# Kernel optimization log

Hardware: AMD Instinct MI355X
Metric: run time of the kernel (lower is better)

Reference implementation:

```python
import jax, jax.numpy as jnp
import numpy as np

N, E, S = 50000, 800000, 3          # nodes, edges, message-passing steps
ND, ED, GD = 7, 4, 2                # raw node/edge/global feature dims
H, L = 64, 64                       # hidden and latent sizes


def _mlp3(x, W0, b0, W1, b1, W2, b2):
    # MLP([H, H, L]) with gelu between layers, none after last (dropout off).
    x = jax.nn.gelu(x @ W0 + b0)
    x = jax.nn.gelu(x @ W1 + b1)
    return x @ W2 + b2


def _ln(x, scale, bias, eps=1e-6):
    mu = jnp.mean(x, axis=-1, keepdims=True)
    xc = x - mu
    var = jnp.mean(xc * xc, axis=-1, keepdims=True)
    return xc * jax.lax.rsqrt(var + eps) * scale + bias


def setup_inputs() -> dict:
    key = jax.random.key(0)
    ks = iter(jax.random.split(key, 40))

    def W(i, o, stacked=False):
        shape = (S, i, o) if stacked else (i, o)
        return (jax.random.normal(next(ks), shape, jnp.float32) / np.sqrt(i)).astype(jnp.float32)

    inp = {
        "nodes": jax.random.normal(next(ks), (N, ND), jnp.float32),
        "edges": jax.random.normal(next(ks), (E, ED), jnp.float32),
        "glob": jax.random.normal(next(ks), (1, GD), jnp.float32),
        # node embedder MLP [H,H,L]
        "emb_n_W0": W(ND, H), "emb_n_b0": jnp.zeros((H,), jnp.float32),
        "emb_n_W1": W(H, H), "emb_n_b1": jnp.zeros((H,), jnp.float32),
        "emb_n_W2": W(H, L), "emb_n_b2": jnp.zeros((L,), jnp.float32),
        # edge embedder MLP
        "emb_e_W0": W(ED, H), "emb_e_b0": jnp.zeros((H,), jnp.float32),
        "emb_e_W1": W(H, H), "emb_e_b1": jnp.zeros((H,), jnp.float32),
        "emb_e_W2": W(H, L), "emb_e_b2": jnp.zeros((L,), jnp.float32),
        # per-step edge update MLP: in = edges(L)+senders(L)+receivers(L)+glob(GD)
        "edge_W0": W(3 * L + GD, H, True), "edge_b0": jnp.zeros((S, H), jnp.float32),
        "edge_W1": W(H, H, True), "edge_b1": jnp.zeros((S, H), jnp.float32),
        "edge_W2": W(H, L, True), "edge_b2": jnp.zeros((S, L), jnp.float32),
        # per-step node update MLP: in = nodes(L)+received(L)+glob(GD)
        "node_W0": W(2 * L + GD, H, True), "node_b0": jnp.zeros((S, H), jnp.float32),
        "node_W1": W(H, H, True), "node_b1": jnp.zeros((S, H), jnp.float32),
        "node_W2": W(H, L, True), "node_b2": jnp.zeros((S, L), jnp.float32),
        # per-step LayerNorms for nodes and edges
        "ln_n_scale": jnp.ones((S, L), jnp.float32), "ln_n_bias": jnp.zeros((S, L), jnp.float32),
        "ln_e_scale": jnp.ones((S, L), jnp.float32), "ln_e_bias": jnp.zeros((S, L), jnp.float32),
        # decoder MLP [H,H,3]
        "dec_W0": W(L, H), "dec_b0": jnp.zeros((H,), jnp.float32),
        "dec_W1": W(H, H), "dec_b1": jnp.zeros((H,), jnp.float32),
        "dec_W2": W(H, 3), "dec_b2": jnp.zeros((3,), jnp.float32),
        "senders": jax.random.randint(next(ks), (E,), 0, N),
        "receivers": jax.random.randint(next(ks), (E,), 0, N),
    }
    return inp


def reference(nodes, edges, glob,
              emb_n_W0, emb_n_b0, emb_n_W1, emb_n_b1, emb_n_W2, emb_n_b2,
              emb_e_W0, emb_e_b0, emb_e_W1, emb_e_b1, emb_e_W2, emb_e_b2,
              edge_W0, edge_b0, edge_W1, edge_b1, edge_W2, edge_b2,
              node_W0, node_b0, node_W1, node_b1, node_W2, node_b2,
              ln_n_scale, ln_n_bias, ln_e_scale, ln_e_bias,
              dec_W0, dec_b0, dec_W1, dec_b1, dec_W2, dec_b2,
              senders, receivers):
    # GraphMapFeatures embedder
    n = _mlp3(nodes, emb_n_W0, emb_n_b0, emb_n_W1, emb_n_b1, emb_n_W2, emb_n_b2)  # [N, L]
    e = _mlp3(edges, emb_e_W0, emb_e_b0, emb_e_W1, emb_e_b1, emb_e_W2, emb_e_b2)  # [E, L]
    n_nodes, n_edges = n.shape[0], e.shape[0]
    ge = jnp.broadcast_to(glob, (n_edges, glob.shape[1]))  # globals per edge (single graph)
    gn = jnp.broadcast_to(glob, (n_nodes, glob.shape[1]))  # globals per node
    steps = edge_W0.shape[0]
    for s in range(steps):
        # edge update: gather sender/receiver node feats, concat, MLP
        e_in = jnp.concatenate([e, n[senders], n[receivers], ge], axis=1)  # [E, 3L+GD]
        new_e = _mlp3(e_in, edge_W0[s], edge_b0[s], edge_W1[s], edge_b1[s], edge_W2[s], edge_b2[s])
        # scatter-aggregate to receivers (jraph default: segment_sum)
        recv = jax.ops.segment_sum(new_e, receivers, num_segments=n_nodes)  # [N, L]
        n_in = jnp.concatenate([n, recv, gn], axis=1)  # [N, 2L+GD]
        new_n = _mlp3(n_in, node_W0[s], node_b0[s], node_W1[s], node_b1[s], node_W2[s], node_b2[s])
        # residual skip connections then per-step LayerNorm
        n = _ln(n + new_n, ln_n_scale[s], ln_n_bias[s])
        e = _ln(e + new_e, ln_e_scale[s], ln_e_bias[s])
    # decoder on nodes -> [N, 3]
    return _mlp3(n, dec_W0, dec_b0, dec_W1, dec_b1, dec_W2, dec_b2)
```

## Files before the change

kernel.cpp:

```cpp
#include <hip/hip_runtime.h>

#define N_NODES 50000
#define N_EDGES 800000
#define NSTEPS 3
#define NBLK_SCAN 196

typedef __attribute__((ext_vector_type(8))) short bf16x8;
typedef __attribute__((ext_vector_type(4))) float f32x4;


__device__ __forceinline__ float ldf(const void* p, long i, int bf) {
    if (bf) {
        unsigned int u = ((const unsigned short*)p)[i];
        u <<= 16;
        return __uint_as_float(u);
    }
    return ((const float*)p)[i];
}

__device__ __forceinline__ unsigned short f2bf(float f) {
    return (unsigned short)((__float_as_uint(f) + 0x8000u) >> 16);
}

__device__ __forceinline__ float bf2f(unsigned short u) {
    return __uint_as_float(((unsigned int)u) << 16);
}

__device__ __forceinline__ float gelu_f(float x) {
    float x2 = x * x;
    float m = x * fmaf(-0.10294325f, x2, -2.30220847f);
    float e = __builtin_amdgcn_exp2f(m);
    return x * __builtin_amdgcn_rcpf(1.0f + e);
}

__device__ __forceinline__ void zero4(f32x4 a[4]) {
#pragma unroll
    for (int t = 0; t < 4; t++) a[t] = (f32x4){0.f, 0.f, 0.f, 0.f};
}

__device__ __forceinline__ void mfma_chunk(f32x4 acc[4], bf16x8 a, const unsigned short* bb) {
    acc[0] = __builtin_amdgcn_mfma_f32_16x16x32_bf16(a, *(const bf16x8*)(bb + 0), acc[0], 0, 0, 0);
    acc[1] = __builtin_amdgcn_mfma_f32_16x16x32_bf16(a, *(const bf16x8*)(bb + 512), acc[1], 0, 0, 0);
    acc[2] = __builtin_amdgcn_mfma_f32_16x16x32_bf16(a, *(const bf16x8*)(bb + 1024), acc[2], 0, 0, 0);
    acc[3] = __builtin_amdgcn_mfma_f32_16x16x32_bf16(a, *(const bf16x8*)(bb + 1536), acc[3], 0, 0, 0);
}

__global__ void detect_kernel(const void* probe, int* flag) {
    if (threadIdx.x == 0 && blockIdx.x == 0) {
        unsigned int w = *(const unsigned int*)probe;
        *flag = (w == 0x3F803F80u) ? 1 : 0;
    }
}

__global__ void hist_kernel(const int* __restrict__ receivers, int* __restrict__ counts) {
    int i = blockIdx.x * 256 + threadIdx.x;
    if (i < N_EDGES) atomicAdd(&counts[receivers[i]], 1);
}

__global__ void scan_partial(const int* __restrict__ counts, int* __restrict__ base,
                             int* __restrict__ blockSums) {
    __shared__ int sm[256];
    int b = blockIdx.x, t = threadIdx.x, i = b * 256 + t;
    int v = (i < N_NODES) ? counts[i] : 0;
    sm[t] = v;
    __syncthreads();
    for (int off = 1; off < 256; off <<= 1) {
        int x = (t >= off) ? sm[t - off] : 0;
        __syncthreads();
        sm[t] += x;
        __syncthreads();
    }
    if (i < N_NODES) base[i] = sm[t] - v;
    if (t == 255) blockSums[b] = sm[255];
}

__global__ void scan_tops(int* __restrict__ blockSums, int* __restrict__ tops) {
    __shared__ int sm[256];
    int t = threadIdx.x;
    int v = (t < NBLK_SCAN) ? blockSums[t] : 0;
    sm[t] = v;
    __syncthreads();
    for (int off = 1; off < 256; off <<= 1) {
        int x = (t >= off) ? sm[t - off] : 0;
        __syncthreads();
        sm[t] += x;
        __syncthreads();
    }
    if (t < NBLK_SCAN) tops[t] = sm[t] - v;
}

__global__ void scan_add(int* __restrict__ base, const int* __restrict__ tops,
                         int* __restrict__ cursor) {
    int b = blockIdx.x, i = b * 256 + threadIdx.x;
    if (i < N_NODES) {
        int v = base[i] + tops[b];
        base[i] = v;
        cursor[i] = v;
    }
}

__global__ void scatter_kernel(const int* __restrict__ senders,
                               const int* __restrict__ receivers, int* __restrict__ cursor,
                               int* __restrict__ ss, int* __restrict__ rsrt,
                               int* __restrict__ perm) {
    int i = blockIdx.x * 256 + threadIdx.x;
    if (i < N_EDGES) {
        int r = receivers[i];
        int pos = atomicAdd(&cursor[r], 1);
        ss[pos] = senders[i];
        rsrt[pos] = r;
        perm[pos] = i;
    }
}

struct PrepPtrs {
    const void* W[14];
    const void* eb0;
    const void* nb0;
    const void* glob;
};

#define PREP_WTOTAL 139264
__global__ void prep_all(PrepPtrs p, unsigned short* WbBase, float* b0eff_e, float* b0eff_n,
                         const int* __restrict__ flagp) {
    const int totals[14] = {36864, 12288, 12288, 24576, 12288, 12288, 2048,
                            4096,  4096,  2048,  4096,  4096,  4096,  4096};
    const int ksrc[14] = {192, 64, 64, 128, 64, 64, 7, 64, 64, 4, 64, 64, 64, 64};
    const int sstride[14] = {12416, 4096, 4096, 8320, 4096, 4096, 448,
                             4096,  4096, 256,  4096, 4096, 4096, 4096};
    const int nch[14] = {6, 2, 2, 4, 2, 2, 1, 2, 2, 1, 2, 2, 2, 2};

    const int bf = *flagp;
    int i = blockIdx.x * 256 + threadIdx.x;
    if (i < PREP_WTOTAL) {
        int e = 0, base = 0;
        while (i >= base + totals[e]) { base += totals[e]; e++; }
        int il = i - base;
        int j = il & 7, lane = (il >> 3) & 63, t = (il >> 9) & 3;
        int c = (il >> 11) % nch[e], s = il / (2048 * nch[e]);
        int k = c * 32 + (lane >> 4) * 8 + j;
        int col = t * 16 + (lane & 15);
        WbBase[i] = (k < ksrc[e]) ? f2bf(ldf(p.W[e], (long)s * sstride[e] + (long)k * 64 + col, bf))
                                  : (unsigned short)0;
    } else if (i < PREP_WTOTAL + 384) {
        int i2 = i - PREP_WTOTAL;
        float g0 = ldf(p.glob, 0, bf), g1 = ldf(p.glob, 1, bf);
        if (i2 < 192) {
            int s = i2 >> 6, col = i2 & 63;
            b0eff_e[i2] = ldf(p.eb0, i2, bf) + g0 * ldf(p.W[0], (long)s * 12416 + 192 * 64 + col, bf)
                                             + g1 * ldf(p.W[0], (long)s * 12416 + 193 * 64 + col, bf);
        } else {
            int il = i2 - 192;
            int s = il >> 6, col = il & 63;
            b0eff_n[il] = ldf(p.nb0, il, bf) + g0 * ldf(p.W[3], (long)s * 8320 + 128 * 64 + col, bf)
                                             + g1 * ldf(p.W[3], (long)s * 8320 + 129 * 64 + col, bf);
        }
    }
}

template <int DIN, int OUT_BF>
__global__ __launch_bounds__(256) void embed_mfma(
    const void* __restrict__ xin, const unsigned short* __restrict__ Wb0, const void* b0,
    const unsigned short* __restrict__ Wb1, const void* b1,
    const unsigned short* __restrict__ Wb2, const void* b2, void* __restrict__ outp,
    unsigned short* __restrict__ out_bf, const int* __restrict__ perm, int R,
    const int* __restrict__ flagp) {
    __shared__ __align__(16) unsigned short Xs[64 * 40];
    __shared__ __align__(16) unsigned short hbuf[64 * 72];
    const int bf = *flagp;
    const int tid = threadIdx.x;
    const long rb = (long)blockIdx.x * 64;
    const int lane = tid & 63, w = tid >> 6, q = lane >> 4, l15 = lane & 15;
    const int arow = 16 * w + l15, aoff = q * 8;
    unsigned short* hw = hbuf + w * 16 * 72;

    {
        int r = tid >> 2, seg = tid & 3;
        long idx = rb + r;
        long src = (perm != nullptr && idx < R) ? (long)perm[idx] : idx;
        unsigned short u[8];
#pragma unroll
        for (int j = 0; j < 8; j++) {
            int col = seg * 8 + j;
            u[j] = (col < DIN && idx < R) ? f2bf(ldf(xin, src * DIN + col, bf)) : (unsigned short)0;
        }
        *(uint4*)&Xs[r * 40 + seg * 8] = *(uint4*)u;
    }

    f32x4 acc[4];
    zero4(acc);
    {
        bf16x8 a = *(const bf16x8*)&Xs[arow * 40 + aoff];
        mfma_chunk(acc, a, Wb0 + lane * 8);
#pragma unroll
        for (int t = 0; t < 4; t++) {
            int col = t * 16 + l15;
            float b = ldf(b0, col, bf);
#pragma unroll
            for (int reg = 0; reg < 4; reg++)
                hw[(q * 4 + reg) * 72 + col] = f2bf(gelu_f(acc[t][reg] + b));
        }
    }
    zero4(acc);
    {
#pragma unroll
        for (int c = 0; c < 2; c++) {
            bf16x8 a = *(const bf16x8*)&hw[l15 * 72 + c * 32 + aoff];
            mfma_chunk(acc, a, Wb1 + c * 2048 + lane * 8);
        }
#pragma unroll
        for (int t = 0; t < 4; t++) {
            int col = t * 16 + l15;
            float b = ldf(b1, col, bf);
#pragma unroll
            for (int reg = 0; reg < 4; reg++)
                hw[(q * 4 + reg) * 72 + col] = f2bf(gelu_f(acc[t][reg] + b));
        }
    }
    zero4(acc);
    {
#pragma unroll
        for (int c = 0; c < 2; c++) {
            bf16x8 a = *(const bf16x8*)&hw[l15 * 72 + c * 32 + aoff];
            mfma_chunk(acc, a, Wb2 + c * 2048 + lane * 8);
        }
    }
    if (OUT_BF) {
#pragma unroll
        for (int t = 0; t < 4; t++) {
            int col = t * 16 + l15;
            float b = ldf(b2, col, bf);
#pragma unroll
            for (int reg = 0; reg < 4; reg++)
                hw[(q * 4 + reg) * 72 + col] = f2bf(acc[t][reg] + b);
        }
#pragma unroll
        for (int p = 0; p < 2; p++) {
            int r = 16 * w + p * 8 + (lane >> 3), o = lane & 7;
            long idx = rb + r;
            if (idx < R)
                *(uint4*)&((unsigned short*)outp)[idx * 64 + o * 8] =
                    *(const uint4*)&hbuf[r * 72 + o * 8];
        }
    } else {
#pragma unroll
        for (int t = 0; t < 4; t++) {
            int col = t * 16 + l15;
            float b = ldf(b2, col, bf);
#pragma unroll
            for (int reg = 0; reg < 4; reg++) {
                long idx = rb + 16 * w + q * 4 + reg;
                if (idx < R) {
                    float v = acc[t][reg] + b;
                    ((float*)outp)[idx * 64 + col] = v;
                    out_bf[idx * 64 + col] = f2bf(v);
                }
            }
        }
    }
}

#define EST 72
#define NST 68
__global__ __launch_bounds__(256) void edge_update_mfma(
    unsigned short* __restrict__ e_lat, const unsigned short* __restrict__ n_bf,
    const int* __restrict__ ss, const int* __restrict__ rsrt,
    const unsigned short* __restrict__ Wb0, const unsigned short* __restrict__ Wb1,
    const unsigned short* __restrict__ Wb2, const float* __restrict__ b0eff, const void* b1,
    const void* b2, const void* lnsc, const void* lnbi, float* __restrict__ recvbuf, int s,
    const int* __restrict__ flagp) {
    __shared__ __align__(16) unsigned short Ee[64 * EST];
    __shared__ __align__(16) unsigned short NsNr[128 * NST];
    __shared__ int rcvs[64];
    float* newe = (float*)NsNr;

    const int bf = *flagp;
    const int tid = threadIdx.x;
    const long rb = (long)blockIdx.x * 64;
    const int lane = tid & 63, w = tid >> 6, q = lane >> 4, l15 = lane & 15;
    const int arow = 16 * w + l15, aoff = q * 8;
    unsigned short* hw = Ee + w * 16 * EST;

#pragma unroll
    for (int p = 0; p < 2; p++) {
        int r = 16 * w + p * 8 + (lane >> 3), o = lane & 7;
        *(uint4*)&Ee[r * EST + o * 8] = ((const uint4*)(e_lat + (rb + r) * 64))[o];
    }
#pragma unroll
    for (int p = 0; p < 2; p++) {
        int r = 16 * w + p * 8 + (lane >> 3), o = lane & 7;
        long node = ss[rb + r];
        *(uint4*)&NsNr[r * NST + o * 8] = ((const uint4*)(n_bf + node * 64))[o];
    }
#pragma unroll
    for (int p = 0; p < 2; p++) {
        int r = 16 * w + p * 8 + (lane >> 3), o = lane & 7;
        long node = rsrt[rb + r];
        *(uint4*)&NsNr[(64 + r) * NST + o * 8] = ((const uint4*)(n_bf + node * 64))[o];
    }
    if (lane < 16) rcvs[16 * w + lane] = rsrt[rb + 16 * w + lane];

    float ein[4][4];
#pragma unroll
    for (int reg = 0; reg < 4; reg++)
#pragma unroll
        for (int t = 0; t < 4; t++)
            ein[reg][t] = bf2f(Ee[(16 * w + q * 4 + reg) * EST + t * 16 + l15]);

    f32x4 acc[4];
    zero4(acc);
    {
        const unsigned short* B = Wb0 + (long)s * 6 * 2048 + lane * 8;
#pragma unroll
        for (int c = 0; c < 2; c++) {
            bf16x8 a = *(const bf16x8*)&Ee[arow * EST + c * 32 + aoff];
            mfma_chunk(acc, a, B + c * 2048);
        }
#pragma unroll
        for (int c = 0; c < 2; c++) {
            bf16x8 a = *(const bf16x8*)&NsNr[arow * NST + c * 32 + aoff];
            mfma_chunk(acc, a, B + (2 + c) * 2048);
        }
#pragma unroll
        for (int c = 0; c < 2; c++) {
            bf16x8 a = *(const bf16x8*)&NsNr[(64 + arow) * NST + c * 32 + aoff];
            mfma_chunk(acc, a, B + (4 + c) * 2048);
        }
#pragma unroll
        for (int t = 0; t < 4; t++) {
            const int col = t * 16 + l15;
            const float b = b0eff[s * 64 + col];
#pragma unroll
            for (int reg = 0; reg < 4; reg++)
                hw[(q * 4 + reg) * EST + col] = f2bf(gelu_f(acc[t][reg] + b));
        }
    }
    zero4(acc);
    {
        const unsigned short* B = Wb1 + (long)s * 2 * 2048 + lane * 8;
#pragma unroll
        for (int c = 0; c < 2; c++) {
            bf16x8 a = *(const bf16x8*)&hw[l15 * EST + c * 32 + aoff];
            mfma_chunk(acc, a, B + c * 2048);
        }
#pragma unroll
        for (int t = 0; t < 4; t++) {
            const int col = t * 16 + l15;
            const float b = ldf(b1, (long)s * 64 + col, bf);
#pragma unroll
            for (int reg = 0; reg < 4; reg++)
                hw[(q * 4 + reg) * EST + col] = f2bf(gelu_f(acc[t][reg] + b));
        }
    }
    zero4(acc);
    {
        const unsigned short* B = Wb2 + (long)s * 2 * 2048 + lane * 8;
#pragma unroll
        for (int c = 0; c < 2; c++) {
            bf16x8 a = *(const bf16x8*)&hw[l15 * EST + c * 32 + aoff];
            mfma_chunk(acc, a, B + c * 2048);
        }
    }
    __syncthreads();

    float fin[4][4];
#pragma unroll
    for (int t = 0; t < 4; t++) {
        const float b = ldf(b2, (long)s * 64 + t * 16 + l15, bf);
#pragma unroll
        for (int reg = 0; reg < 4; reg++) fin[reg][t] = acc[t][reg] + b;
    }
    float lsc[4], lbi[4];
#pragma unroll
    for (int t = 0; t < 4; t++) {
        lsc[t] = ldf(lnsc, (long)s * 64 + t * 16 + l15, bf);
        lbi[t] = ldf(lnbi, (long)s * 64 + t * 16 + l15, bf);
    }
#pragma unroll
    for (int reg = 0; reg < 4; reg++) {
        const int lr = q * 4 + reg;
        float u[4], ssum = 0.f;
#pragma unroll
        for (int t = 0; t < 4; t++) {
            newe[w * 1056 + lr * 66 + t * 16 + l15] = fin[reg][t];
            u[t] = ein[reg][t] + fin[reg][t];
            ssum += u[t];
        }
#pragma unroll
        for (int m = 1; m < 16; m <<= 1) ssum += __shfl_xor(ssum, m, 64);
        const float mu = ssum * (1.0f / 64.0f);
        float d[4], vv = 0.f;
#pragma unroll
        for (int t = 0; t < 4; t++) { d[t] = u[t] - mu; vv += d[t] * d[t]; }
#pragma unroll
        for (int m = 1; m < 16; m <<= 1) vv += __shfl_xor(vv, m, 64);
        const float rs = rsqrtf(vv * (1.0f / 64.0f) + 1e-6f);
#pragma unroll
        for (int t = 0; t < 4; t++)
            Ee[(16 * w + lr) * EST + t * 16 + l15] = f2bf(d[t] * rs * lsc[t] + lbi[t]);
    }

#pragma unroll
    for (int p = 0; p < 2; p++) {
        int r = 16 * w + p * 8 + (lane >> 3), o = lane & 7;
        *(uint4*)&e_lat[(rb + r) * 64 + o * 8] = *(const uint4*)&Ee[r * EST + o * 8];
    }
    {
        const int col = tid & 63, g = tid >> 6;
        float a = 0.f;
#pragma unroll
        for (int rr = 0; rr < 16; rr++) {
            const int r = 16 * g + rr;
            a += newe[g * 1056 + rr * 66 + col];
            if (rr == 15 || rcvs[r + 1] != rcvs[r]) {
                atomicAdd(&recvbuf[(long)rcvs[r] * 64 + col], a);
                a = 0.f;
            }
        }
    }
}

#define NXS 136
__global__ __launch_bounds__(256) void node_update_mfma(
    float* __restrict__ n_lat, unsigned short* __restrict__ n_bf, float* __restrict__ recvbuf,
    const unsigned short* __restrict__ Wb0, const float* __restrict__ b0eff,
    const unsigned short* __restrict__ Wb1, const void* b1,
    const unsigned short* __restrict__ Wb2, const void* b2, const void* lnsc,
    const void* lnbi, int s, const int* __restrict__ flagp) {
    __shared__ __align__(16) unsigned short Xs[64 * NXS];
    __shared__ __align__(16) unsigned short hbuf[64 * 72];
    const int bf = *flagp;
    const int tid = threadIdx.x;
    const long rb = (long)blockIdx.x * 64;
    const int lane = tid & 63, w = tid >> 6, q = lane >> 4, l15 = lane & 15;
    const int arow = 16 * w + l15, aoff = q * 8;
    unsigned short* hw = hbuf + w * 16 * 72;

#pragma unroll
    for (int p = 0; p < 2; p++) {
        int r = 16 * w + p * 8 + (lane >> 3), o = lane & 7;
        long idx = rb + r;
        uint4 v = {0u, 0u, 0u, 0u};
        if (idx < N_NODES) v = ((const uint4*)(n_bf + idx * 64))[o];
        *(uint4*)&Xs[r * NXS + o * 8] = v;
    }
#pragma unroll
    for (int p = 0; p < 2; p++) {
        int r = 16 * w + p * 8 + (lane >> 3), o = lane & 7;
        long idx = rb + r;
        unsigned short u[8] = {0, 0, 0, 0, 0, 0, 0, 0};
        if (idx < N_NODES) {
            const float* src = recvbuf + idx * 64 + o * 8;
            float4 x0 = *(const float4*)src, x1 = *(const float4*)(src + 4);
            u[0] = f2bf(x0.x); u[1] = f2bf(x0.y); u[2] = f2bf(x0.z); u[3] = f2bf(x0.w);
            u[4] = f2bf(x1.x); u[5] = f2bf(x1.y); u[6] = f2bf(x1.z); u[7] = f2bf(x1.w);
        }
        *(uint4*)&Xs[r * NXS + 64 + o * 8] = *(uint4*)u;
    }

    f32x4 acc[4];
    zero4(acc);
    {
        const unsigned short* B = Wb0 + (long)s * 4 * 2048 + lane * 8;
#pragma unroll
        for (int c = 0; c < 4; c++) {
            bf16x8 a = *(const bf16x8*)&Xs[arow * NXS + c * 32 + aoff];
            mfma_chunk(acc, a, B + c * 2048);
        }
#pragma unroll
        for (int t = 0; t < 4; t++) {
            const int col = t * 16 + l15;
            const float b = b0eff[s * 64 + col];
#pragma unroll
            for (int reg = 0; reg < 4; reg++)
                hw[(q * 4 + reg) * 72 + col] = f2bf(gelu_f(acc[t][reg] + b));
        }
    }
    zero4(acc);
    {
        const unsigned short* B = Wb1 + (long)s * 2 * 2048 + lane * 8;
#pragma unroll
        for (int c = 0; c < 2; c++) {
            bf16x8 a = *(const bf16x8*)&hw[l15 * 72 + c * 32 + aoff];
            mfma_chunk(acc, a, B + c * 2048);
        }
#pragma unroll
        for (int t = 0; t < 4; t++) {
            const int col = t * 16 + l15;
            const float b = ldf(b1, (long)s * 64 + col, bf);
#pragma unroll
            for (int reg = 0; reg < 4; reg++)
                hw[(q * 4 + reg) * 72 + col] = f2bf(gelu_f(acc[t][reg] + b));
        }
    }
    zero4(acc);
    {
        const unsigned short* B = Wb2 + (long)s * 2 * 2048 + lane * 8;
#pragma unroll
        for (int c = 0; c < 2; c++) {
            bf16x8 a = *(const bf16x8*)&hw[l15 * 72 + c * 32 + aoff];
            mfma_chunk(acc, a, B + c * 2048);
        }
    }
    float b2v[4], lsc[4], lbi[4];
#pragma unroll
    for (int t = 0; t < 4; t++) {
        b2v[t] = ldf(b2, (long)s * 64 + t * 16 + l15, bf);
        lsc[t] = ldf(lnsc, (long)s * 64 + t * 16 + l15, bf);
        lbi[t] = ldf(lnbi, (long)s * 64 + t * 16 + l15, bf);
    }
#pragma unroll
    for (int reg = 0; reg < 4; reg++) {
        const int rowl = 16 * w + q * 4 + reg;
        const long idx = rb + rowl;
        const bool valid = idx < N_NODES;
        float u[4], ssum = 0.f;
#pragma unroll
        for (int t = 0; t < 4; t++) {
            const int col = t * 16 + l15;
            float xn = valid ? n_lat[idx * 64 + col] : 0.f;
            u[t] = xn + acc[t][reg] + b2v[t];
            ssum += u[t];
        }
#pragma unroll
        for (int m = 1; m < 16; m <<= 1) ssum += __shfl_xor(ssum, m, 64);
        const float mu = ssum * (1.0f / 64.0f);
        float d[4], vv = 0.f;
#pragma unroll
        for (int t = 0; t < 4; t++) { d[t] = u[t] - mu; vv += d[t] * d[t]; }
#pragma unroll
        for (int m = 1; m < 16; m <<= 1) vv += __shfl_xor(vv, m, 64);
        const float rs = rsqrtf(vv * (1.0f / 64.0f) + 1e-6f);
        if (valid) {
#pragma unroll
            for (int t = 0; t < 4; t++) {
                const int col = t * 16 + l15;
                float v = d[t] * rs * lsc[t] + lbi[t];
                n_lat[idx * 64 + col] = v;
                n_bf[idx * 64 + col] = f2bf(v);
                recvbuf[idx * 64 + col] = 0.f;
            }
        }
    }
}

__global__ __launch_bounds__(256) void decoder_mfma(
    const unsigned short* __restrict__ n_bf, const unsigned short* __restrict__ Wb0,
    const void* b0, const unsigned short* __restrict__ Wb1, const void* b1, const void* W2,
    const void* b2, void* __restrict__ outp, const int* __restrict__ flagp) {
    __shared__ __align__(16) unsigned short Xs[64 * 72];
    __shared__ __align__(16) unsigned short hbuf[64 * 72];
    const int bf = *flagp;
    const int tid = threadIdx.x;
    const long rb = (long)blockIdx.x * 64;
    const int lane = tid & 63, w = tid >> 6, q = lane >> 4, l15 = lane & 15;
    const int arow = 16 * w + l15, aoff = q * 8;
    unsigned short* hw = hbuf + w * 16 * 72;

#pragma unroll
    for (int p = 0; p < 2; p++) {
        int r = 16 * w + p * 8 + (lane >> 3), o = lane & 7;
        long idx = rb + r;
        uint4 v = {0u, 0u, 0u, 0u};
        if (idx < N_NODES) v = ((const uint4*)(n_bf + idx * 64))[o];
        *(uint4*)&Xs[r * 72 + o * 8] = v;
    }

    f32x4 acc[4];
    zero4(acc);
    {
#pragma unroll
        for (int c = 0; c < 2; c++) {
            bf16x8 a = *(const bf16x8*)&Xs[arow * 72 + c * 32 + aoff];
            mfma_chunk(acc, a, Wb0 + c * 2048 + lane * 8);
        }
#pragma unroll
        for (int t = 0; t < 4; t++) {
            const int col = t * 16 + l15;
            const float b = ldf(b0, col, bf);
#pragma unroll
            for (int reg = 0; reg < 4; reg++)
                hw[(q * 4 + reg) * 72 + col] = f2bf(gelu_f(acc[t][reg] + b));
        }
    }
    zero4(acc);
    {
#pragma unroll
        for (int c = 0; c < 2; c++) {
            bf16x8 a = *(const bf16x8*)&hw[l15 * 72 + c * 32 + aoff];
            mfma_chunk(acc, a, Wb1 + c * 2048 + lane * 8);
        }
#pragma unroll
        for (int t = 0; t < 4; t++) {
            const int col = t * 16 + l15;
            const float b = ldf(b1, col, bf);
#pragma unroll
            for (int reg = 0; reg < 4; reg++)
                hw[(q * 4 + reg) * 72 + col] = f2bf(gelu_f(acc[t][reg] + b));
        }
    }
    const int col = tid & 63;
    const int r0 = (tid >> 6) * 16;
    if (col < 3) {
        float a[16];
        const float b = ldf(b2, col, bf);
#pragma unroll
        for (int i = 0; i < 16; i++) a[i] = b;
        for (int k = 0; k < 64; k++) {
            float wv = ldf(W2, (long)k * 3 + col, bf);
#pragma unroll
            for (int i = 0; i < 16; i++) a[i] = fmaf(bf2f(hbuf[(r0 + i) * 72 + k]), wv, a[i]);
        }
        for (int i = 0; i < 16; i++) {
            const long idx = rb + r0 + i;
            if (idx < N_NODES) {
                if (bf)
                    ((unsigned short*)outp)[idx * 3 + col] = f2bf(a[i]);
                else
                    ((float*)outp)[idx * 3 + col] = a[i];
            }
        }
    }
}

extern "C" void kernel_launch(void* const* d_in, const int* in_sizes, int n_in, void* d_out,
                              int out_size, void* d_ws, size_t ws_size, hipStream_t stream) {
    const void* nodes = d_in[0];
    const void* edges = d_in[1];
    const void* glob = d_in[2];
    const void *enW0 = d_in[3], *enb0 = d_in[4], *enW1 = d_in[5], *enb1 = d_in[6],
               *enW2 = d_in[7], *enb2 = d_in[8];
    const void *eeW0 = d_in[9], *eeb0 = d_in[10], *eeW1 = d_in[11], *eeb1 = d_in[12],
               *eeW2 = d_in[13], *eeb2 = d_in[14];
    const void *eW0 = d_in[15], *eb0 = d_in[16], *eW1 = d_in[17], *eb1 = d_in[18],
               *eW2 = d_in[19], *eb2 = d_in[20];
    const void *nW0 = d_in[21], *nb0 = d_in[22], *nW1 = d_in[23], *nb1 = d_in[24],
               *nW2 = d_in[25], *nb2 = d_in[26];
    const void *lnns = d_in[27], *lnnb = d_in[28], *lnes = d_in[29], *lneb = d_in[30];
    const void *dW0 = d_in[31], *db0 = d_in[32], *dW1 = d_in[33], *db1 = d_in[34],
               *dW2 = d_in[35], *db2 = d_in[36];
    const int* senders = (const int*)d_in[37];
    const int* receivers = (const int*)d_in[38];

    float* n_lat = (float*)d_ws;
    float* recvb = n_lat + 3200000;
    float* b0eff_e = recvb + 3200000;
    float* b0eff_n = b0eff_e + 192;
    int* flag = (int*)(b0eff_n + 192);
    unsigned short* e_lat = (unsigned short*)(b0eff_n + 256);
    unsigned short* n_bf = e_lat + 51200000;
    unsigned short* WbBase = n_bf + 3200000;
    unsigned short* WbE0 = WbBase;
    unsigned short* WbE1 = WbBase + 36864;
    unsigned short* WbE2 = WbBase + 49152;
    unsigned short* WbN0 = WbBase + 61440;
    unsigned short* WbN1 = WbBase + 86016;
    unsigned short* WbN2 = WbBase + 98304;
    unsigned short* WbNE0 = WbBase + 110592;
    unsigned short* WbNE1 = WbBase + 112640;
    unsigned short* WbNE2 = WbBase + 116736;
    unsigned short* WbEE0 = WbBase + 120832;
    unsigned short* WbEE1 = WbBase + 122880;
    unsigned short* WbEE2 = WbBase + 126976;
    unsigned short* WbD0 = WbBase + 131072;
    unsigned short* WbD1 = WbBase + 135168;
    int* counts = (int*)(WbBase + 139264 + 64);
    int* sbase = counts + N_NODES;
    int* cursor = sbase + N_NODES;
    int* blockSums = cursor + N_NODES;
    int* tops = blockSums + 256;
    int* ss = tops + 256;
    int* rsrt = ss + N_EDGES;
    int* perm = rsrt + N_EDGES;

    detect_kernel<<<1, 64, 0, stream>>>(lnns, flag);

    PrepPtrs pp;
    pp.W[0] = eW0;  pp.W[1] = eW1;  pp.W[2] = eW2;
    pp.W[3] = nW0;  pp.W[4] = nW1;  pp.W[5] = nW2;
    pp.W[6] = enW0; pp.W[7] = enW1; pp.W[8] = enW2;
    pp.W[9] = eeW0; pp.W[10] = eeW1; pp.W[11] = eeW2;
    pp.W[12] = dW0; pp.W[13] = dW1;
    pp.eb0 = eb0; pp.nb0 = nb0; pp.glob = glob;
    prep_all<<<(PREP_WTOTAL + 384 + 255) / 256, 256, 0, stream>>>(pp, WbBase, b0eff_e, b0eff_n,
                                                                  flag);
    hipMemsetAsync(recvb, 0, (size_t)N_NODES * 64 * sizeof(float), stream);
    hipMemsetAsync(counts, 0, (size_t)N_NODES * sizeof(int), stream);

    hist_kernel<<<(N_EDGES + 255) / 256, 256, 0, stream>>>(receivers, counts);
    scan_partial<<<NBLK_SCAN, 256, 0, stream>>>(counts, sbase, blockSums);
    scan_tops<<<1, 256, 0, stream>>>(blockSums, tops);
    scan_add<<<NBLK_SCAN, 256, 0, stream>>>(sbase, tops, cursor);
    scatter_kernel<<<(N_EDGES + 255) / 256, 256, 0, stream>>>(senders, receivers, cursor, ss,
                                                              rsrt, perm);

    embed_mfma<7, 0><<<(N_NODES + 63) / 64, 256, 0, stream>>>(
        nodes, WbNE0, enb0, WbNE1, enb1, WbNE2, enb2, n_lat, n_bf, (const int*)nullptr,
        N_NODES, flag);
    embed_mfma<4, 1><<<N_EDGES / 64, 256, 0, stream>>>(
        edges, WbEE0, eeb0, WbEE1, eeb1, WbEE2, eeb2, e_lat, (unsigned short*)nullptr, perm,
        N_EDGES, flag);
    for (int s = 0; s < NSTEPS; s++) {
        edge_update_mfma<<<N_EDGES / 64, 256, 0, stream>>>(
            e_lat, n_bf, ss, rsrt, WbE0, WbE1, WbE2, b0eff_e, eb1, eb2, lnes, lneb, recvb, s,
            flag);
        node_update_mfma<<<(N_NODES + 63) / 64, 256, 0, stream>>>(
            n_lat, n_bf, recvb, WbN0, b0eff_n, WbN1, nb1, WbN2, nb2, lnns, lnnb, s, flag);
    }
    decoder_mfma<<<(N_NODES + 63) / 64, 256, 0, stream>>>(n_bf, WbD0, db0, WbD1, db1, dW2,
                                                          db2, d_out, flag);
}
```

Before: 772.9 us.

## Fuse edge embedder into first edge step and decoder into last node step

The edge embedding MLP now runs inside the first edge-update kernel, so the embedded edge latents are never written to and re-read from global memory. The final edge step skips its LayerNorm and e_lat write-back, since those edge latents are never used again. The decoder is folded into the last node-update kernel. Sender and receiver node features are now loaded straight into MFMA operand registers instead of being staged through shared memory, which frees LDS and removes a __syncthreads. The cost is more template variants and higher register pressure in the fused kernels.

```diff
diff --git a/kernel.cpp b/kernel.cpp
--- a/kernel.cpp
+++ b/kernel.cpp
@@ -261,18 +261,20 @@
 }
 
 #define EST 72
-#define NST 68
-__global__ __launch_bounds__(256) void edge_update_mfma(
+template <int S0, int LAST>
+__global__ __launch_bounds__(256) void edge_step(
     unsigned short* __restrict__ e_lat, const unsigned short* __restrict__ n_bf,
-    const int* __restrict__ ss, const int* __restrict__ rsrt,
+    const int* __restrict__ ss, const int* __restrict__ rsrt, const int* __restrict__ perm,
+    const void* __restrict__ xe_raw, const unsigned short* __restrict__ We0, const void* eb0_,
+    const unsigned short* __restrict__ We1, const void* eb1_,
+    const unsigned short* __restrict__ We2, const void* eb2_,
     const unsigned short* __restrict__ Wb0, const unsigned short* __restrict__ Wb1,
     const unsigned short* __restrict__ Wb2, const float* __restrict__ b0eff, const void* b1,
     const void* b2, const void* lnsc, const void* lnbi, float* __restrict__ recvbuf, int s,
     const int* __restrict__ flagp) {
     __shared__ __align__(16) unsigned short Ee[64 * EST];
-    __shared__ __align__(16) unsigned short NsNr[128 * NST];
+    __shared__ __align__(16) float newe[4 * 1056];
     __shared__ int rcvs[64];
-    float* newe = (float*)NsNr;
 
     const int bf = *flagp;
     const int tid = threadIdx.x;
@@ -281,33 +283,86 @@
     const int arow = 16 * w + l15, aoff = q * 8;
     unsigned short* hw = Ee + w * 16 * EST;
 
-#pragma unroll
-    for (int p = 0; p < 2; p++) {
-        int r = 16 * w + p * 8 + (lane >> 3), o = lane & 7;
-        *(uint4*)&Ee[r * EST + o * 8] = ((const uint4*)(e_lat + (rb + r) * 64))[o];
-    }
-#pragma unroll
-    for (int p = 0; p < 2; p++) {
-        int r = 16 * w + p * 8 + (lane >> 3), o = lane & 7;
-        long node = ss[rb + r];
-        *(uint4*)&NsNr[r * NST + o * 8] = ((const uint4*)(n_bf + node * 64))[o];
-    }
-#pragma unroll
-    for (int p = 0; p < 2; p++) {
-        int r = 16 * w + p * 8 + (lane >> 3), o = lane & 7;
-        long node = rsrt[rb + r];
-        *(uint4*)&NsNr[(64 + r) * NST + o * 8] = ((const uint4*)(n_bf + node * 64))[o];
-    }
+    const int sn = ss[rb + arow], rn = rsrt[rb + arow];
+    const bf16x8 as0 = *(const bf16x8*)(n_bf + (long)sn * 64 + aoff);
+    const bf16x8 as1 = *(const bf16x8*)(n_bf + (long)sn * 64 + 32 + aoff);
+    const bf16x8 ar0 = *(const bf16x8*)(n_bf + (long)rn * 64 + aoff);
+    const bf16x8 ar1 = *(const bf16x8*)(n_bf + (long)rn * 64 + 32 + aoff);
     if (lane < 16) rcvs[16 * w + lane] = rsrt[rb + 16 * w + lane];
 
     float ein[4][4];
-#pragma unroll
-    for (int reg = 0; reg < 4; reg++)
-#pragma unroll
-        for (int t = 0; t < 4; t++)
-            ein[reg][t] = bf2f(Ee[(16 * w + q * 4 + reg) * EST + t * 16 + l15]);
-
     f32x4 acc[4];
+
+    if (S0) {
+        zero4(acc);
+        {
+            bf16x8 a = (bf16x8){0, 0, 0, 0, 0, 0, 0, 0};
+            if (q == 0) {
+                long src = perm[rb + arow];
+                unsigned short u[8] = {0, 0, 0, 0, 0, 0, 0, 0};
+#pragma unroll
+                for (int j = 0; j < 4; j++) u[j] = f2bf(ldf(xe_raw, src * 4 + j, bf));
+                a = *(const bf16x8*)u;
+            }
+            mfma_chunk(acc, a, We0 + lane * 8);
+#pragma unroll
+            for (int t = 0; t < 4; t++) {
+                int col = t * 16 + l15;
+                float b = ldf(eb0_, col, bf);
+#pragma unroll
+                for (int reg = 0; reg < 4; reg++)
+                    hw[(q * 4 + reg) * EST + col] = f2bf(gelu_f(acc[t][reg] + b));
+            }
+        }
+        zero4(acc);
+        {
+#pragma unroll
+            for (int c = 0; c < 2; c++) {
+                bf16x8 a = *(const bf16x8*)&hw[l15 * EST + c * 32 + aoff];
+                mfma_chunk(acc, a, We1 + c * 2048 + lane * 8);
+            }
+#pragma unroll
+            for (int t = 0; t < 4; t++) {
+                int col = t * 16 + l15;
+                float b = ldf(eb1_, col, bf);
+#pragma unroll
+                for (int reg = 0; reg < 4; reg++)
+                    hw[(q * 4 + reg) * EST + col] = f2bf(gelu_f(acc[t][reg] + b));
+            }
+        }
+        zero4(acc);
+        {
+#pragma unroll
+            for (int c = 0; c < 2; c++) {
+                bf16x8 a = *(const bf16x8*)&hw[l15 * EST + c * 32 + aoff];
+                mfma_chunk(acc, a, We2 + c * 2048 + lane * 8);
+            }
+#pragma unroll
+            for (int t = 0; t < 4; t++) {
+                int col = t * 16 + l15;
+                float b = ldf(eb2_, col, bf);
+#pragma unroll
+                for (int reg = 0; reg < 4; reg++) {
+                    ein[reg][t] = acc[t][reg] + b;
+                    Ee[(16 * w + q * 4 + reg) * EST + col] = f2bf(ein[reg][t]);
+                }
+            }
+        }
+    } else {
+#pragma unroll
+        for (int p = 0; p < 2; p++) {
+            int r = 16 * w + p * 8 + (lane >> 3), o = lane & 7;
+            *(uint4*)&Ee[r * EST + o * 8] = ((const uint4*)(e_lat + (rb + r) * 64))[o];
+        }
+        if (!LAST) {
+#pragma unroll
+            for (int reg = 0; reg < 4; reg++)
+#pragma unroll
+                for (int t = 0; t < 4; t++)
+                    ein[reg][t] = bf2f(Ee[(16 * w + q * 4 + reg) * EST + t * 16 + l15]);
+        }
+    }
+
     zero4(acc);
     {
         const unsigned short* B = Wb0 + (long)s * 6 * 2048 + lane * 8;
@@ -316,16 +371,10 @@
             bf16x8 a = *(const bf16x8*)&Ee[arow * EST + c * 32 + aoff];
             mfma_chunk(acc, a, B + c * 2048);
         }
-#pragma unroll
-        for (int c = 0; c < 2; c++) {
-            bf16x8 a = *(const bf16x8*)&NsNr[arow * NST + c * 32 + aoff];
-            mfma_chunk(acc, a, B + (2 + c) * 2048);
-        }
-#pragma unroll
-        for (int c = 0; c < 2; c++) {
-            bf16x8 a = *(const bf16x8*)&NsNr[(64 + arow) * NST + c * 32 + aoff];
-            mfma_chunk(acc, a, B + (4 + c) * 2048);
-        }
+        mfma_chunk(acc, as0, B + 2 * 2048);
+        mfma_chunk(acc, as1, B + 3 * 2048);
+        mfma_chunk(acc, ar0, B + 4 * 2048);
+        mfma_chunk(acc, ar1, B + 5 * 2048);
 #pragma unroll
         for (int t = 0; t < 4; t++) {
             const int col = t * 16 + l15;
@@ -361,7 +410,6 @@
             mfma_chunk(acc, a, B + c * 2048);
         }
     }
-    __syncthreads();
 
     float fin[4][4];
 #pragma unroll
@@ -371,39 +419,46 @@
         for (int reg = 0; reg < 4; reg++) fin[reg][t] = acc[t][reg] + b;
     }
     float lsc[4], lbi[4];
-#pragma unroll
-    for (int t = 0; t < 4; t++) {
-        lsc[t] = ldf(lnsc, (long)s * 64 + t * 16 + l15, bf);
-        lbi[t] = ldf(lnbi, (long)s * 64 + t * 16 + l15, bf);
+    if (!LAST) {
+#pragma unroll
+        for (int t = 0; t < 4; t++) {
+            lsc[t] = ldf(lnsc, (long)s * 64 + t * 16 + l15, bf);
+            lbi[t] = ldf(lnbi, (long)s * 64 + t * 16 + l15, bf);
+        }
     }
 #pragma unroll
     for (int reg = 0; reg < 4; reg++) {
         const int lr = q * 4 + reg;
-        float u[4], ssum = 0.f;
-#pragma unroll
-        for (int t = 0; t < 4; t++) {
-            newe[w * 1056 + lr * 66 + t * 16 + l15] = fin[reg][t];
-            u[t] = ein[reg][t] + fin[reg][t];
-            ssum += u[t];
-        }
-#pragma unroll
-        for (int m = 1; m < 16; m <<= 1) ssum += __shfl_xor(ssum, m, 64);
-        const float mu = ssum * (1.0f / 64.0f);
-        float d[4], vv = 0.f;
-#pragma unroll
-        for (int t = 0; t < 4; t++) { d[t] = u[t] - mu; vv += d[t] * d[t]; }
-#pragma unroll
-        for (int m = 1; m < 16; m <<= 1) vv += __shfl_xor(vv, m, 64);
-        const float rs = rsqrtf(vv * (1.0f / 64.0f) + 1e-6f);
-#pragma unroll
-        for (int t = 0; t < 4; t++)
-            Ee[(16 * w + lr) * EST + t * 16 + l15] = f2bf(d[t] * rs * lsc[t] + lbi[t]);
-    }
-
-#pragma unroll
-    for (int p = 0; p < 2; p++) {
-        int r = 16 * w + p * 8 + (lane >> 3), o = lane & 7;
-        *(uint4*)&e_lat[(rb + r) * 64 + o * 8] = *(const uint4*)&Ee[r * EST + o * 8];
+#pragma unroll
+        for (int t = 0; t < 4; t++) newe[w * 1056 + lr * 66 + t * 16 + l15] = fin[reg][t];
+        if (!LAST) {
+            float u[4], ssum = 0.f;
+#pragma unroll
+            for (int t = 0; t < 4; t++) {
+                u[t] = ein[reg][t] + fin[reg][t];
+                ssum += u[t];
+            }
+#pragma unroll
+            for (int m = 1; m < 16; m <<= 1) ssum += __shfl_xor(ssum, m, 64);
+            const float mu = ssum * (1.0f / 64.0f);
+            float d[4], vv = 0.f;
+#pragma unroll
+            for (int t = 0; t < 4; t++) { d[t] = u[t] - mu; vv += d[t] * d[t]; }
+#pragma unroll
+            for (int m = 1; m < 16; m <<= 1) vv += __shfl_xor(vv, m, 64);
+            const float rs = rsqrtf(vv * (1.0f / 64.0f) + 1e-6f);
+#pragma unroll
+            for (int t = 0; t < 4; t++)
+                Ee[(16 * w + lr) * EST + t * 16 + l15] = f2bf(d[t] * rs * lsc[t] + lbi[t]);
+        }
+    }
+
+    if (!LAST) {
+#pragma unroll
+        for (int p = 0; p < 2; p++) {
+            int r = 16 * w + p * 8 + (lane >> 3), o = lane & 7;
+            *(uint4*)&e_lat[(rb + r) * 64 + o * 8] = *(const uint4*)&Ee[r * EST + o * 8];
+        }
     }
     {
         const int col = tid & 63, g = tid >> 6;
@@ -421,12 +476,15 @@
 }
 
 #define NXS 136
+template <int FINAL>
 __global__ __launch_bounds__(256) void node_update_mfma(
     float* __restrict__ n_lat, unsigned short* __restrict__ n_bf, float* __restrict__ recvbuf,
     const unsigned short* __restrict__ Wb0, const float* __restrict__ b0eff,
     const unsigned short* __restrict__ Wb1, const void* b1,
     const unsigned short* __restrict__ Wb2, const void* b2, const void* lnsc,
-    const void* lnbi, int s, const int* __restrict__ flagp) {
+    const void* lnbi, const unsigned short* __restrict__ WbD0, const void* db0,
+    const unsigned short* __restrict__ WbD1, const void* db1, const void* dW2,
+    const void* db2, void* __restrict__ outp, int s, const int* __restrict__ flagp) {
     __shared__ __align__(16) unsigned short Xs[64 * NXS];
     __shared__ __align__(16) unsigned short hbuf[64 * 72];
     const int bf = *flagp;
@@ -531,7 +589,13 @@
 #pragma unroll
         for (int m = 1; m < 16; m <<= 1) vv += __shfl_xor(vv, m, 64);
         const float rs = rsqrtf(vv * (1.0f / 64.0f) + 1e-6f);
-        if (valid) {
+        if (FINAL) {
+#pragma unroll
+            for (int t = 0; t < 4; t++) {
+                const int col = t * 16 + l15;
+                hw[(q * 4 + reg) * 72 + col] = f2bf(d[t] * rs * lsc[t] + lbi[t]);
+            }
+        } else if (valid) {
 #pragma unroll
             for (int t = 0; t < 4; t++) {
                 const int col = t * 16 + l15;
@@ -542,82 +606,59 @@
             }
         }
     }
-}
-
-__global__ __launch_bounds__(256) void decoder_mfma(
-    const unsigned short* __restrict__ n_bf, const unsigned short* __restrict__ Wb0,
-    const void* b0, const unsigned short* __restrict__ Wb1, const void* b1, const void* W2,
-    const void* b2, void* __restrict__ outp, const int* __restrict__ flagp) {
-    __shared__ __align__(16) unsigned short Xs[64 * 72];
-    __shared__ __align__(16) unsigned short hbuf[64 * 72];
-    const int bf = *flagp;
-    const int tid = threadIdx.x;
-    const long rb = (long)blockIdx.x * 64;
-    const int lane = tid & 63, w = tid >> 6, q = lane >> 4, l15 = lane & 15;
-    const int arow = 16 * w + l15, aoff = q * 8;
-    unsigned short* hw = hbuf + w * 16 * 72;
-
-#pragma unroll
-    for (int p = 0; p < 2; p++) {
-        int r = 16 * w + p * 8 + (lane >> 3), o = lane & 7;
-        long idx = rb + r;
-        uint4 v = {0u, 0u, 0u, 0u};
-        if (idx < N_NODES) v = ((const uint4*)(n_bf + idx * 64))[o];
-        *(uint4*)&Xs[r * 72 + o * 8] = v;
-    }
-
-    f32x4 acc[4];
-    zero4(acc);
-    {
-#pragma unroll
-        for (int c = 0; c < 2; c++) {
-            bf16x8 a = *(const bf16x8*)&Xs[arow * 72 + c * 32 + aoff];
-            mfma_chunk(acc, a, Wb0 + c * 2048 + lane * 8);
-        }
-#pragma unroll
-        for (int t = 0; t < 4; t++) {
-            const int col = t * 16 + l15;
-            const float b = ldf(b0, col, bf);
-#pragma unroll
-            for (int reg = 0; reg < 4; reg++)
-                hw[(q * 4 + reg) * 72 + col] = f2bf(gelu_f(acc[t][reg] + b));
-        }
-    }
-    zero4(acc);
-    {
-#pragma unroll
-        for (int c = 0; c < 2; c++) {
-            bf16x8 a = *(const bf16x8*)&hw[l15 * 72 + c * 32 + aoff];
-            mfma_chunk(acc, a, Wb1 + c * 2048 + lane * 8);
-        }
-#pragma unroll
-        for (int t = 0; t < 4; t++) {
-            const int col = t * 16 + l15;
-            const float b = ldf(b1, col, bf);
-#pragma unroll
-            for (int reg = 0; reg < 4; reg++)
-                hw[(q * 4 + reg) * 72 + col] = f2bf(gelu_f(acc[t][reg] + b));
-        }
-    }
-    const int col = tid & 63;
-    const int r0 = (tid >> 6) * 16;
-    if (col < 3) {
-        float a[16];
-        const float b = ldf(b2, col, bf);
-#pragma unroll
-        for (int i = 0; i < 16; i++) a[i] = b;
-        for (int k = 0; k < 64; k++) {
-            float wv = ldf(W2, (long)k * 3 + col, bf);
-#pragma unroll
-            for (int i = 0; i < 16; i++) a[i] = fmaf(bf2f(hbuf[(r0 + i) * 72 + k]), wv, a[i]);
-        }
-        for (int i = 0; i < 16; i++) {
-            const long idx = rb + r0 + i;
-            if (idx < N_NODES) {
-                if (bf)
-                    ((unsigned short*)outp)[idx * 3 + col] = f2bf(a[i]);
-                else
-                    ((float*)outp)[idx * 3 + col] = a[i];
+    if (FINAL) {
+        zero4(acc);
+        {
+#pragma unroll
+            for (int c = 0; c < 2; c++) {
+                bf16x8 a = *(const bf16x8*)&hw[l15 * 72 + c * 32 + aoff];
+                mfma_chunk(acc, a, WbD0 + c * 2048 + lane * 8);
+            }
+#pragma unroll
+            for (int t = 0; t < 4; t++) {
+                const int col = t * 16 + l15;
+                const float b = ldf(db0, col, bf);
+#pragma unroll
+                for (int reg = 0; reg < 4; reg++)
+                    hw[(q * 4 + reg) * 72 + col] = f2bf(gelu_f(acc[t][reg] + b));
+            }
+        }
+        zero4(acc);
+        {
+#pragma unroll
+            for (int c = 0; c < 2; c++) {
+                bf16x8 a = *(const bf16x8*)&hw[l15 * 72 + c * 32 + aoff];
+                mfma_chunk(acc, a, WbD1 + c * 2048 + lane * 8);
+            }
+#pragma unroll
+            for (int t = 0; t < 4; t++) {
+                const int col = t * 16 + l15;
+                const float b = ldf(db1, col, bf);
+#pragma unroll
+                for (int reg = 0; reg < 4; reg++)
+                    hw[(q * 4 + reg) * 72 + col] = f2bf(gelu_f(acc[t][reg] + b));
+            }
+        }
+        const int col = tid & 63;
+        const int r0 = w * 16;
+        if (col < 3) {
+            float a[16];
+            const float b = ldf(db2, col, bf);
+#pragma unroll
+            for (int i = 0; i < 16; i++) a[i] = b;
+            for (int k = 0; k < 64; k++) {
+                float wv = ldf(dW2, (long)k * 3 + col, bf);
+#pragma unroll
+                for (int i = 0; i < 16; i++) a[i] = fmaf(bf2f(hw[i * 72 + k]), wv, a[i]);
+            }
+            for (int i = 0; i < 16; i++) {
+                const long idx = rb + r0 + i;
+                if (idx < N_NODES) {
+                    if (bf)
+                        ((unsigned short*)outp)[idx * 3 + col] = f2bf(a[i]);
+                    else
+                        ((float*)outp)[idx * 3 + col] = a[i];
+                }
             }
         }
     }
@@ -697,16 +738,25 @@
     embed_mfma<7, 0><<<(N_NODES + 63) / 64, 256, 0, stream>>>(
         nodes, WbNE0, enb0, WbNE1, enb1, WbNE2, enb2, n_lat, n_bf, (const int*)nullptr,
         N_NODES, flag);
-    embed_mfma<4, 1><<<N_EDGES / 64, 256, 0, stream>>>(
-        edges, WbEE0, eeb0, WbEE1, eeb1, WbEE2, eeb2, e_lat, (unsigned short*)nullptr, perm,
-        N_EDGES, flag);
-    for (int s = 0; s < NSTEPS; s++) {
-        edge_update_mfma<<<N_EDGES / 64, 256, 0, stream>>>(
-            e_lat, n_bf, ss, rsrt, WbE0, WbE1, WbE2, b0eff_e, eb1, eb2, lnes, lneb, recvb, s,
-            flag);
-        node_update_mfma<<<(N_NODES + 63) / 64, 256, 0, stream>>>(
-            n_lat, n_bf, recvb, WbN0, b0eff_n, WbN1, nb1, WbN2, nb2, lnns, lnnb, s, flag);
-    }
-    decoder_mfma<<<(N_NODES + 63) / 64, 256, 0, stream>>>(n_bf, WbD0, db0, WbD1, db1, dW2,
-                                                          db2, d_out, flag);
-}
+
+    edge_step<1, 0><<<N_EDGES / 64, 256, 0, stream>>>(
+        e_lat, n_bf, ss, rsrt, perm, edges, WbEE0, eeb0, WbEE1, eeb1, WbEE2, eeb2,
+        WbE0, WbE1, WbE2, b0eff_e, eb1, eb2, lnes, lneb, recvb, 0, flag);
+    node_update_mfma<0><<<(N_NODES + 63) / 64, 256, 0, stream>>>(
+        n_lat, n_bf, recvb, WbN0, b0eff_n, WbN1, nb1, WbN2, nb2, lnns, lnnb,
+        nullptr, nullptr, nullptr, nullptr, nullptr, nullptr, nullptr, 0, flag);
+
+    edge_step<0, 0><<<N_EDGES / 64, 256, 0, stream>>>(
+        e_lat, n_bf, ss, rsrt, perm, edges, WbEE0, eeb0, WbEE1, eeb1, WbEE2, eeb2,
+        WbE0, WbE1, WbE2, b0eff_e, eb1, eb2, lnes, lneb, recvb, 1, flag);
+    node_update_mfma<0><<<(N_NODES + 63) / 64, 256, 0, stream>>>(
+        n_lat, n_bf, recvb, WbN0, b0eff_n, WbN1, nb1, WbN2, nb2, lnns, lnnb,
+        nullptr, nullptr, nullptr, nullptr, nullptr, nullptr, nullptr, 1, flag);
+
+    edge_step<0, 1><<<N_EDGES / 64, 256, 0, stream>>>(
+        e_lat, n_bf, ss, rsrt, perm, edges, WbEE0, eeb0, WbEE1, eeb1, WbEE2, eeb2,
+        WbE0, WbE1, WbE2, b0eff_e, eb1, eb2, lnes, lneb, recvb, 2, flag);
+    node_update_mfma<1><<<(N_NODES + 63) / 64, 256, 0, stream>>>(
+        n_lat, n_bf, recvb, WbN0, b0eff_n, WbN1, nb1, WbN2, nb2, lnns, lnnb,
+        WbD0, db0, WbD1, db1, dW2, db2, d_out, 2, flag);
+}
```

Result: no change. 761.3 us (-1.5%).
